# Performance work log

Hardware: AMD Instinct MI355X
Metric: run time of the kernel (lower is better)

## Reference

```python
import jax, jax.numpy as jnp
import numpy as np

HEAD_COUNT = 16
HEAD_DIM = 128  # embed_count // head_count = 2048 // 16


def setup_inputs() -> dict:
    key = jax.random.key(0)
    k0, k1, k2, k3, k4 = jax.random.split(key, 5)
    B, C, S = 4, 2048, 1024
    keys = jax.random.normal(k0, (B, C, 1, S), dtype=jnp.float32)
    values = jax.random.normal(k1, (B, C, 1, S), dtype=jnp.float32)
    queries = jax.random.normal(k2, (B, C, 1, S), dtype=jnp.float32)
    attention_mask = jax.random.randint(k3, (B, S), 0, 2).astype(bool)
    # guarantee at least one valid key per batch row so softmax is finite
    attention_mask = attention_mask.at[:, 0].set(True)
    w_out = jax.random.normal(k4, (C, C), dtype=jnp.float32) * 0.02
    return {"keys": keys, "values": values, "queries": queries,
            "attention_mask": attention_mask, "w_out": w_out}


def reference(keys, values, queries, attention_mask, w_out):
    B, C, _, S = keys.shape
    h, d = HEAD_COUNT, HEAD_DIM
    # keys: [B,C,1,S] -> transpose(1,3) -> [B,S,1,C] -> [B,S,h,d]
    k = jnp.transpose(keys[:, :, 0, :], (0, 2, 1)).reshape(B, S, h, d)      # bkhd
    # values/queries: [B,C,1,S] -> [B,h,d,S] -> transpose(1,2) -> [B,d,h,S]
    v = jnp.transpose(values[:, :, 0, :].reshape(B, h, d, S), (0, 2, 1, 3))  # bdhk
    q = jnp.transpose(queries[:, :, 0, :].reshape(B, h, d, S), (0, 2, 1, 3)) # bdhq
    # additive mask bias: 0 where attended, -inf where masked; broadcast over h,q
    bias = jnp.where(attention_mask, 0.0, -jnp.inf).astype(keys.dtype)       # [B,K]
    scale = 1.0 / np.sqrt(d).astype(np.float32)
    w = jnp.einsum('bdhq,bkhd->bkhq', q * scale, k)                          # [B,K,h,Q]
    w = w + bias[:, :, None, None]
    w = jax.nn.softmax(w, axis=1)  # softmax over keys (dim 1)
    hid = jnp.einsum('bkhq,bdhk->bdhq', w, v)                                # [B,d,h,Q]
    hid = jnp.transpose(hid, (0, 2, 1, 3)).reshape(B, C, S)                  # [B,C,Q]
    out = jnp.einsum('oc,bcq->boq', w_out, hid)                              # 1x1 conv out_proj
    return out.reshape(B, C, 1, S)
```

## Files before the change

kernel.cpp:

```cpp
#include <hip/hip_runtime.h>

#define Bq 4
#define Cc 2048
#define Ss 1024
#define Hh 16
#define Dd 128

#define QSCALE 0.127517429f

typedef __bf16 bf16x8 __attribute__((ext_vector_type(8)));
typedef float  f32x4  __attribute__((ext_vector_type(4)));

__device__ __forceinline__ ushort f2bf(float f) {
    uint u = __float_as_uint(f);
    u += 0x7FFFu + ((u >> 16) & 1u);
    return (ushort)(u >> 16);
}
__device__ __forceinline__ uint pack2bf(float a, float b) {
    return (uint)f2bf(a) | ((uint)f2bf(b) << 16);
}
__device__ __forceinline__ void gld16(const void* g, void* l) {
    __builtin_amdgcn_global_load_lds(
        (const __attribute__((address_space(1))) unsigned int*)g,
        (__attribute__((address_space(3))) unsigned int*)l, 16, 0, 0);
}

__global__ __launch_bounds__(256) void prep_all2(const float* __restrict__ w,
                                                 const float* __restrict__ v,
                                                 const float* __restrict__ keys,
                                                 const float* __restrict__ queries,
                                                 const unsigned* __restrict__ mask,
                                                 ushort* __restrict__ wb,
                                                 ushort* __restrict__ vb,
                                                 ushort* __restrict__ Kt,
                                                 ushort* __restrict__ Qt,
                                                 float* __restrict__ bias) {
    __shared__ __align__(16) float T[128][65];
    const int t = threadIdx.x;
    const int blk = blockIdx.x;

    if (blk < 2048) {
        const size_t e = ((size_t)blk * 256 + t) * 8;
        const int row = (int)(e >> 11), col = (int)(e & 2047);
        const int colS = (col & ~63) | ((col & 63) ^ ((row & 7) << 3));
        float4 v0 = *(const float4*)&w[e];
        float4 v1 = *(const float4*)&w[e + 4];
        uint4 o;
        o.x = pack2bf(v0.x, v0.y); o.y = pack2bf(v0.z, v0.w);
        o.z = pack2bf(v1.x, v1.y); o.w = pack2bf(v1.z, v1.w);
        *(uint4*)&wb[(size_t)row * 2048 + colS] = o;
    } else if (blk < 6144) {
        const int tid = (blk - 2048) * 256 + t;
        const int row = tid >> 7;
        const int cp = tid & 127;
        const int blk64 = (cp >> 3) * 64;
        const int j0 = cp & 7;
        const int b5 = j0 >> 2, h = j0 & 3;
        const float* src = v + (size_t)row * 1024 + blk64 + 32 * b5 + 4 * h;
        float4 A = *(const float4*)src;
        float4 B = *(const float4*)(src + 16);
        uint4 o;
        o.x = pack2bf(A.x, A.y); o.y = pack2bf(A.z, A.w);
        o.z = pack2bf(B.x, B.y); o.w = pack2bf(B.z, B.w);
        *(uint4*)&vb[(size_t)row * 1024 + blk64 + ((j0 * 8) ^ ((row & 7) << 3))] = o;
    } else if (blk < 8192) {
        const int isQ = (blk >= 7168);
        const int b2 = blk - (isQ ? 7168 : 6144);
        const int s0 = (b2 & 15) * 64;
        const int bh = b2 >> 4;
        const float* src = (isQ ? queries : keys) + (size_t)bh * 128 * 1024;
        const float sc = isQ ? QSCALE : 1.0f;
#pragma unroll
        for (int p = 0; p < 8; ++p) {
            const int d = p * 16 + (t >> 4);
            float4 v4 = *(const float4*)&src[(size_t)d * 1024 + s0 + (t & 15) * 4];
            T[d][(t & 15) * 4 + 0] = v4.x * sc;
            T[d][(t & 15) * 4 + 1] = v4.y * sc;
            T[d][(t & 15) * 4 + 2] = v4.z * sc;
            T[d][(t & 15) * 4 + 3] = v4.w * sc;
        }
        __syncthreads();
        ushort* outp = isQ ? Qt : Kt;
#pragma unroll
        for (int p = 0; p < 4; ++p) {
            const int k = p * 16 + (t >> 4);
            const int x = t & 15;
            uint4 o;
            o.x = pack2bf(T[x * 8 + 0][k], T[x * 8 + 1][k]);
            o.y = pack2bf(T[x * 8 + 2][k], T[x * 8 + 3][k]);
            o.z = pack2bf(T[x * 8 + 4][k], T[x * 8 + 5][k]);
            o.w = pack2bf(T[x * 8 + 6][k], T[x * 8 + 7][k]);
            const size_t rowbyte = ((size_t)bh * 1024 + s0 + k) * 256;
            const int boff = isQ ? (x * 16) : ((x * 16) ^ ((k & 7) << 4));
            *(uint4*)((char*)outp + rowbyte + boff) = o;
        }
    } else {
        __shared__ int f01, ff;
        if (t == 0) { f01 = 0; ff = 0; }
        __syncthreads();
        int a = 0, c = 0;
        for (int i = t; i < 1024; i += 256) {
            unsigned vv = mask[i];
            if (vv != 0u && vv != 1u) a = 1;
            if (vv != 0u && vv != 0x3F800000u) c = 1;
        }
        if (a) atomicOr(&f01, 1);
        if (c) atomicOr(&ff, 1);
        __syncthreads();
        const int mode = f01 ? (ff ? 1 : 2) : 0;
        const int* mi = (const int*)mask;
        const unsigned char* mb = (const unsigned char*)mask;
        const float* mf = (const float*)mask;
        for (int i = t; i < Bq * Ss; i += 256) {
            bool on;
            if (mode == 0)      on = (mi[i] != 0);
            else if (mode == 1) on = (mb[i] != 0);
            else                on = (mf[i] != 0.0f);
            bias[i] = on ? 0.0f : -1e30f;
        }
    }
}

__global__ __launch_bounds__(512) void attn9(const ushort* __restrict__ Qt,
                                             const ushort* __restrict__ Kt,
                                             const ushort* __restrict__ Vbf,
                                             const float* __restrict__ bias,
                                             ushort* __restrict__ hidT) {
    __shared__ __align__(16) char SMEM[69632];
    float* biasS = (float*)(SMEM + 65536);

    const int t = threadIdx.x, l = t & 63, w = t >> 6;
    const int kk = l & 15, g = l >> 4;

    const int bid = blockIdx.x;
    const int vid = (bid & 7) * 32 + (bid >> 3);
    const int bh = vid >> 2, qt = vid & 3;
    const int b = bh >> 4, hh = bh & 15;
    const int q0 = qt * 256;
    const size_t bhbase = (size_t)bh * 1024;

    for (int i = t; i < Ss; i += 512) biasS[i] = bias[b * Ss + i];

    bf16x8 qf[2][4];
#pragma unroll
    for (int qs = 0; qs < 2; ++qs) {
        const ushort* qrow = Qt + (bhbase + q0 + w * 32 + qs * 16 + kk) * 128;
#pragma unroll
        for (int dc = 0; dc < 4; ++dc)
            qf[qs][dc] = *(const bf16x8*)(qrow + dc * 32 + g * 8);
    }

    float lrun[2] = {0.0f, 0.0f};
    f32x4 hacc[2][8];
#pragma unroll
    for (int qs = 0; qs < 2; ++qs)
#pragma unroll
        for (int i = 0; i < 8; ++i) hacc[qs][i] = (f32x4){0.f, 0.f, 0.f, 0.f};

#define ATTN_STAGE(bufi, cki)                                                   \
    {                                                                           \
        const int k0n = (cki) * 64;                                             \
        ushort* Kd = (ushort*)SMEM + (bufi) * 8192;                             \
        ushort* Vd = (ushort*)(SMEM + 32768) + (bufi) * 8192;                   \
        _Pragma("unroll")                                                       \
        for (int ii = 0; ii < 4; ++ii) {                                        \
            const int inst = ii * 8 + w;                                        \
            if (inst < 16) {                                                    \
                gld16(Kt + (bhbase + k0n + inst * 4 + (l >> 4)) * 128 +         \
                          (l & 15) * 8,                                         \
                      Kd + inst * 512);                                         \
            } else {                                                            \
                const int i2 = inst - 16;                                       \
                gld16(Vbf + ((size_t)bh * 128 + i2 * 8 + (l >> 3)) * 1024 +     \
                          k0n + (l & 7) * 8,                                    \
                      Vd + i2 * 512);                                           \
            }                                                                   \
        }                                                                       \
    }

#define ATTN_COMPUTE(bi, ck)                                                     \
    {                                                                            \
        const int k0 = (ck) * 64;                                                \
        const ushort* KTb = (const ushort*)SMEM + (bi) * 8192;                   \
        const ushort* Vsb = (const ushort*)(SMEM + 32768) + (bi) * 8192;         \
        f32x4 sc[2][4];                                                          \
        __builtin_amdgcn_s_setprio(1);                                           \
        _Pragma("unroll")                                                        \
        for (int ns = 0; ns < 4; ++ns) {                                         \
            const f32x4 ci = *(const f32x4*)&biasS[k0 + ns * 16 + g * 4];        \
            bf16x8 kf[4];                                                        \
            const ushort* kr = KTb + (ns * 16 + kk) * 128;                       \
            _Pragma("unroll")                                                    \
            for (int dc = 0; dc < 4; ++dc)                                       \
                kf[dc] = *(const bf16x8*)(kr +                                   \
                             ((dc * 32 + g * 8) ^ ((kk & 7) << 3)));             \
            _Pragma("unroll")                                                    \
            for (int qs = 0; qs < 2; ++qs) {                                     \
                f32x4 a = ci;                                                    \
                _Pragma("unroll")                                                \
                for (int dc = 0; dc < 4; ++dc)                                   \
                    a = __builtin_amdgcn_mfma_f32_16x16x32_bf16(                 \
                        kf[dc], qf[qs][dc], a, 0, 0, 0);                         \
                sc[qs][ns] = a;                                                  \
            }                                                                    \
        }                                                                        \
        __builtin_amdgcn_s_setprio(0);                                           \
        bf16x8 pb[2][2];                                                         \
        _Pragma("unroll")                                                        \
        for (int qs = 0; qs < 2; ++qs) {                                         \
            float pv[4][4];                                                      \
            float s = 0.0f;                                                      \
            _Pragma("unroll")                                                    \
            for (int ns = 0; ns < 4; ++ns) {                                     \
                _Pragma("unroll")                                                \
                for (int r = 0; r < 4; ++r) {                                    \
                    float p = exp2f(sc[qs][ns][r]);                              \
                    pv[ns][r] = p;                                               \
                    s += p;                                                      \
                }                                                                \
            }                                                                    \
            lrun[qs] += s;                                                       \
            _Pragma("unroll")                                                    \
            for (int kh = 0; kh < 2; ++kh) {                                     \
                bf16x8 vpk;                                                      \
                _Pragma("unroll")                                                \
                for (int j = 0; j < 8; ++j)                                      \
                    vpk[j] = (__bf16)pv[2 * kh + (j >> 2)][j & 3];               \
                pb[qs][kh] = vpk;                                                \
            }                                                                    \
        }                                                                        \
        __builtin_amdgcn_s_setprio(1);                                           \
        _Pragma("unroll")                                                        \
        for (int kh = 0; kh < 2; ++kh) {                                         \
            _Pragma("unroll")                                                    \
            for (int ds = 0; ds < 8; ++ds) {                                     \
                bf16x8 vf = *(const bf16x8*)(Vsb + (ds * 16 + kk) * 64 +         \
                                 ((kh * 32 + g * 8) ^ ((kk & 7) << 3)));         \
                hacc[0][ds] = __builtin_amdgcn_mfma_f32_16x16x32_bf16(           \
                    vf, pb[0][kh], hacc[0][ds], 0, 0, 0);                        \
                hacc[1][ds] = __builtin_amdgcn_mfma_f32_16x16x32_bf16(           \
                    vf, pb[1][kh], hacc[1][ds], 0, 0, 0);                        \
            }                                                                    \
        }                                                                        \
        __builtin_amdgcn_s_setprio(0);                                           \
    }

    ATTN_STAGE(0, 0);
    asm volatile("s_waitcnt vmcnt(0)" ::: "memory");
    __builtin_amdgcn_s_barrier();

    int buf = 0;
    for (int ck = 0; ck < 16; ++ck) {
        if (ck + 1 < 16) ATTN_STAGE(buf ^ 1, ck + 1);
        ATTN_COMPUTE(buf, ck);
        asm volatile("s_waitcnt vmcnt(0)" ::: "memory");
        __builtin_amdgcn_s_barrier();
        buf ^= 1;
    }
#undef ATTN_STAGE
#undef ATTN_COMPUTE

    float linv[2];
#pragma unroll
    for (int qs = 0; qs < 2; ++qs) {
        float s = lrun[qs];
        s += __shfl_xor(s, 16);
        s += __shfl_xor(s, 32);
        linv[qs] = 1.0f / s;
    }

    __syncthreads();
    {
        ushort* hs = (ushort*)SMEM;
#pragma unroll
        for (int qs = 0; qs < 2; ++qs) {
            const int row = w * 32 + qs * 16 + kk;
#pragma unroll
            for (int ds = 0; ds < 8; ++ds) {
                uint2 pk;
                pk.x = pack2bf(hacc[qs][ds][0] * linv[qs], hacc[qs][ds][1] * linv[qs]);
                pk.y = pack2bf(hacc[qs][ds][2] * linv[qs], hacc[qs][ds][3] * linv[qs]);
                const int off = row * 256 + ((ds * 32 + g * 8) ^ ((row & 7) << 4));
                *(uint2*)((char*)hs + off) = pk;
            }
        }
    }
    __syncthreads();

    const char* hsb = (const char*)SMEM;
#pragma unroll
    for (int it = 0; it < 8; ++it) {
        const int idx = it * 512 + t;
        const int q = idx >> 4, x = idx & 15;
        uint4 vv = *(const uint4*)(hsb + q * 256 + x * 16);
        *(uint4*)((char*)hidT + ((size_t)(b * Ss + q0 + q)) * 4096 + hh * 256 + x * 16) = vv;
    }
}

__global__ __launch_bounds__(512, 2) void proj5(const ushort* __restrict__ Wbf,
                                                const ushort* __restrict__ hidT,
                                                float* __restrict__ out) {
    __shared__ __align__(16) char SMEM[147456];
    const int t = threadIdx.x, l = t & 63, w = t >> 6;
    const int kk = l & 15, g = l >> 4;
    const int wr = w >> 2, wc = w & 3;

    const int bid = blockIdx.x;
    const int vid = (bid & 7) * 32 + (bid >> 3);
    const int o0 = (vid & 15) * 128;
    const int n0 = (vid >> 4) * 256;

    f32x4 acc[4][4];
#pragma unroll
    for (int i = 0; i < 4; ++i)
#pragma unroll
        for (int j = 0; j < 4; ++j) acc[i][j] = (f32x4){0.f, 0.f, 0.f, 0.f};

    const int swz = (kk & 7) << 3;

#define P5_STAGE_A(st, ks)                                                      \
    {                                                                           \
        ushort* Ad = (ushort*)SMEM + (st) * 8192;                               \
        _Pragma("unroll")                                                       \
        for (int ii = 0; ii < 2; ++ii) {                                        \
            const int idx = ii * 512 + t;                                       \
            gld16(Wbf + (size_t)(o0 + (idx >> 3)) * 2048 + (ks) * 64 +          \
                      (idx & 7) * 8,                                            \
                  Ad + idx * 8);                                                \
        }                                                                       \
    }
#define P5_STAGE_B(st, ks, p)                                                   \
    {                                                                           \
        ushort* Bd = (ushort*)(SMEM + 49152) + (st) * 16384;                    \
        _Pragma("unroll")                                                       \
        for (int jj = (p) * 2; jj < (p) * 2 + 2; ++jj) {                        \
            const int idx = jj * 512 + t;                                       \
            gld16(hidT + (size_t)(n0 + (idx >> 3)) * 2048 + (ks) * 64 +         \
                      (idx & 7) * 8,                                            \
                  Bd + idx * 8);                                                \
        }                                                                       \
    }
#define P5_READ(dcv)                                                            \
    _Pragma("unroll")                                                           \
    for (int ms = 0; ms < 4; ++ms)                                              \
        af[ms] = *(const bf16x8*)&Ab[(wr * 64 + ms * 16 + kk) * 64 +            \
                                     (((dcv) * 32 + g * 8) ^ swz)];             \
    _Pragma("unroll")                                                           \
    for (int ns = 0; ns < 4; ++ns)                                              \
        bfr[ns] = *(const bf16x8*)&Bb[(wc * 64 + ns * 16 + kk) * 64 +           \
                                      (((dcv) * 32 + g * 8) ^ swz)];
#define P5_MFMA()                                                               \
    __builtin_amdgcn_s_setprio(1);                                              \
    _Pragma("unroll")                                                           \
    for (int ms = 0; ms < 4; ++ms)                                              \
        _Pragma("unroll")                                                       \
        for (int ns = 0; ns < 4; ++ns)                                          \
            acc[ms][ns] = __builtin_amdgcn_mfma_f32_16x16x32_bf16(              \
                af[ms], bfr[ns], acc[ms][ns], 0, 0, 0);                         \
    __builtin_amdgcn_s_setprio(0);

    P5_STAGE_A(0, 0); P5_STAGE_B(0, 0, 0); P5_STAGE_B(0, 0, 1);
    P5_STAGE_A(1, 1); P5_STAGE_B(1, 1, 0); P5_STAGE_B(1, 1, 1);
    asm volatile("s_waitcnt vmcnt(6)" ::: "memory");
    __builtin_amdgcn_s_barrier();

    int ct = 0, st2 = 2;
    for (int tt = 0; tt < 32; ++tt) {
        const ushort* Ab = (const ushort*)SMEM + ct * 8192;
        const ushort* Bb = (const ushort*)(SMEM + 49152) + ct * 16384;
        bf16x8 af[4], bfr[4];

        P5_READ(0);
        if (tt < 30) { P5_STAGE_A(st2, tt + 2); P5_STAGE_B(st2, tt + 2, 0); }
        __builtin_amdgcn_s_barrier();
        asm volatile("s_waitcnt lgkmcnt(0)" ::: "memory");
        P5_MFMA();
        __builtin_amdgcn_s_barrier();

        P5_READ(1);
        if (tt < 30) P5_STAGE_B(st2, tt + 2, 1);
        if (tt < 30) { asm volatile("s_waitcnt vmcnt(6)" ::: "memory"); }
        else         { asm volatile("s_waitcnt vmcnt(0)" ::: "memory"); }
        __builtin_amdgcn_s_barrier();
        asm volatile("s_waitcnt lgkmcnt(0)" ::: "memory");
        P5_MFMA();
        __builtin_amdgcn_s_barrier();

        ct = (ct == 2) ? 0 : ct + 1;
        st2 = (st2 == 2) ? 0 : st2 + 1;
    }
#undef P5_STAGE_A
#undef P5_STAGE_B
#undef P5_READ
#undef P5_MFMA

#pragma unroll
    for (int ms = 0; ms < 4; ++ms)
#pragma unroll
        for (int ns = 0; ns < 4; ++ns) {
            const int o = o0 + wr * 64 + ms * 16 + g * 4;
            const int n = n0 + wc * 64 + ns * 16 + kk;
            const int bb = n >> 10, qq = n & 1023;
            float* op = out + ((size_t)(bb * Cc + o)) * Ss + qq;
#pragma unroll
            for (int r = 0; r < 4; ++r) op[(size_t)r * Ss] = acc[ms][ns][r];
        }
}

extern "C" void kernel_launch(void* const* d_in, const int* in_sizes, int n_in,
                              void* d_out, int out_size, void* d_ws, size_t ws_size,
                              hipStream_t stream) {
    const float*    keys    = (const float*)d_in[0];
    const float*    values  = (const float*)d_in[1];
    const float*    queries = (const float*)d_in[2];
    const unsigned* mask    = (const unsigned*)d_in[3];
    const float*    w_out   = (const float*)d_in[4];
    float* out = (float*)d_out;

    char* ws = (char*)d_ws;
    float*  bias = (float*)ws;
    ushort* Wbf  = (ushort*)(ws + 16384);
    ushort* Kt   = (ushort*)(ws + 16384 + (8u << 20));
    ushort* Qt   = (ushort*)(ws + 16384 + (24u << 20));
    ushort* Vbf  = (ushort*)(ws + 16384 + (40u << 20));
    ushort* hidT = (ushort*)(ws + 16384 + (56u << 20));

    hipLaunchKernelGGL(prep_all2, dim3(8193), dim3(256), 0, stream,
                       w_out, values, keys, queries, mask,
                       Wbf, Vbf, Kt, Qt, bias);
    hipLaunchKernelGGL(attn9, dim3(256), dim3(512), 0, stream,
                       Qt, Kt, Vbf, bias, hidT);
    hipLaunchKernelGGL(proj5, dim3(256), dim3(512), 0, stream,
                       Wbf, hidT, out);
}
```

Before: 120.9 us.

## Triple-buffer K/V tiles and interleave softmax with PV MFMA in attention

Moves the attention kernel from double to triple buffering of K/V chunks in LDS (shared memory grows to about 100KB), so loads run two chunks ahead and each iteration waits with vmcnt(4) instead of draining all loads. The compute body is also split into halves so softmax of the second half can overlap the PV MFMAs of the first half, and the setprio hints are dropped. The goal is to hide global-load latency and keep the matrix units busier. The cost is more LDS per block, which limits how many blocks fit on a CU.

```diff
diff --git a/kernel.cpp b/kernel.cpp
--- a/kernel.cpp
+++ b/kernel.cpp
@@ -121,13 +121,13 @@
     }
 }
 
-__global__ __launch_bounds__(512) void attn9(const ushort* __restrict__ Qt,
-                                             const ushort* __restrict__ Kt,
-                                             const ushort* __restrict__ Vbf,
-                                             const float* __restrict__ bias,
-                                             ushort* __restrict__ hidT) {
-    __shared__ __align__(16) char SMEM[69632];
-    float* biasS = (float*)(SMEM + 65536);
+__global__ __launch_bounds__(512) void attn10(const ushort* __restrict__ Qt,
+                                              const ushort* __restrict__ Kt,
+                                              const ushort* __restrict__ Vbf,
+                                              const float* __restrict__ bias,
+                                              ushort* __restrict__ hidT) {
+    __shared__ __align__(16) char SMEM[102400];
+    float* biasS = (float*)(SMEM + 98304);
 
     const int t = threadIdx.x, l = t & 63, w = t >> 6;
     const int kk = l & 15, g = l >> 4;
@@ -161,7 +161,7 @@
     {                                                                           \
         const int k0n = (cki) * 64;                                             \
         ushort* Kd = (ushort*)SMEM + (bufi) * 8192;                             \
-        ushort* Vd = (ushort*)(SMEM + 32768) + (bufi) * 8192;                   \
+        ushort* Vd = (ushort*)(SMEM + 49152) + (bufi) * 8192;                   \
         _Pragma("unroll")                                                       \
         for (int ii = 0; ii < 4; ++ii) {                                        \
             const int inst = ii * 8 + w;                                        \
@@ -178,87 +178,95 @@
         }                                                                       \
     }
 
+#define QK_HALF(h)                                                               \
+    _Pragma("unroll")                                                            \
+    for (int n2 = 0; n2 < 2; ++n2) {                                             \
+        const int ns = 2 * (h) + n2;                                             \
+        const f32x4 ci = *(const f32x4*)&biasS[k0 + ns * 16 + g * 4];            \
+        bf16x8 kf[4];                                                            \
+        const ushort* kr = KTb + (ns * 16 + kk) * 128;                           \
+        _Pragma("unroll")                                                        \
+        for (int dc = 0; dc < 4; ++dc)                                           \
+            kf[dc] = *(const bf16x8*)(kr + ((dc * 32 + g * 8) ^ ((kk & 7) << 3)));\
+        _Pragma("unroll")                                                        \
+        for (int qs = 0; qs < 2; ++qs) {                                         \
+            f32x4 a = ci;                                                        \
+            _Pragma("unroll")                                                    \
+            for (int dc = 0; dc < 4; ++dc)                                       \
+                a = __builtin_amdgcn_mfma_f32_16x16x32_bf16(                     \
+                    kf[dc], qf[qs][dc], a, 0, 0, 0);                             \
+            sc[qs][ns] = a;                                                      \
+        }                                                                        \
+    }
+
+#define SM_HALF(h)                                                               \
+    _Pragma("unroll")                                                            \
+    for (int qs = 0; qs < 2; ++qs) {                                             \
+        float pv0[4], pv1[4];                                                    \
+        _Pragma("unroll")                                                        \
+        for (int r = 0; r < 4; ++r) {                                            \
+            pv0[r] = exp2f(sc[qs][2 * (h)][r]);                                  \
+            pv1[r] = exp2f(sc[qs][2 * (h) + 1][r]);                              \
+        }                                                                        \
+        lrun[qs] += (pv0[0] + pv0[1] + pv0[2] + pv0[3])                          \
+                  + (pv1[0] + pv1[1] + pv1[2] + pv1[3]);                         \
+        bf16x8 vpk;                                                              \
+        _Pragma("unroll")                                                        \
+        for (int j = 0; j < 4; ++j) { vpk[j] = (__bf16)pv0[j];                   \
+                                      vpk[j + 4] = (__bf16)pv1[j]; }             \
+        pb[qs][h] = vpk;                                                         \
+    }
+
+#define PV_HALF(h)                                                               \
+    _Pragma("unroll")                                                            \
+    for (int ds = 0; ds < 8; ++ds) {                                             \
+        bf16x8 vf = *(const bf16x8*)(Vsb + (ds * 16 + kk) * 64 +                 \
+                        (((h) * 32 + g * 8) ^ ((kk & 7) << 3)));                 \
+        hacc[0][ds] = __builtin_amdgcn_mfma_f32_16x16x32_bf16(                   \
+            vf, pb[0][h], hacc[0][ds], 0, 0, 0);                                 \
+        hacc[1][ds] = __builtin_amdgcn_mfma_f32_16x16x32_bf16(                   \
+            vf, pb[1][h], hacc[1][ds], 0, 0, 0);                                 \
+    }
+
 #define ATTN_COMPUTE(bi, ck)                                                     \
     {                                                                            \
         const int k0 = (ck) * 64;                                                \
         const ushort* KTb = (const ushort*)SMEM + (bi) * 8192;                   \
-        const ushort* Vsb = (const ushort*)(SMEM + 32768) + (bi) * 8192;         \
+        const ushort* Vsb = (const ushort*)(SMEM + 49152) + (bi) * 8192;         \
         f32x4 sc[2][4];                                                          \
-        __builtin_amdgcn_s_setprio(1);                                           \
-        _Pragma("unroll")                                                        \
-        for (int ns = 0; ns < 4; ++ns) {                                         \
-            const f32x4 ci = *(const f32x4*)&biasS[k0 + ns * 16 + g * 4];        \
-            bf16x8 kf[4];                                                        \
-            const ushort* kr = KTb + (ns * 16 + kk) * 128;                       \
-            _Pragma("unroll")                                                    \
-            for (int dc = 0; dc < 4; ++dc)                                       \
-                kf[dc] = *(const bf16x8*)(kr +                                   \
-                             ((dc * 32 + g * 8) ^ ((kk & 7) << 3)));             \
-            _Pragma("unroll")                                                    \
-            for (int qs = 0; qs < 2; ++qs) {                                     \
-                f32x4 a = ci;                                                    \
-                _Pragma("unroll")                                                \
-                for (int dc = 0; dc < 4; ++dc)                                   \
-                    a = __builtin_amdgcn_mfma_f32_16x16x32_bf16(                 \
-                        kf[dc], qf[qs][dc], a, 0, 0, 0);                         \
-                sc[qs][ns] = a;                                                  \
-            }                                                                    \
-        }                                                                        \
-        __builtin_amdgcn_s_setprio(0);                                           \
         bf16x8 pb[2][2];                                                         \
-        _Pragma("unroll")                                                        \
-        for (int qs = 0; qs < 2; ++qs) {                                         \
-            float pv[4][4];                                                      \
-            float s = 0.0f;                                                      \
-            _Pragma("unroll")                                                    \
-            for (int ns = 0; ns < 4; ++ns) {                                     \
-                _Pragma("unroll")                                                \
-                for (int r = 0; r < 4; ++r) {                                    \
-                    float p = exp2f(sc[qs][ns][r]);                              \
-                    pv[ns][r] = p;                                               \
-                    s += p;                                                      \
-                }                                                                \
-            }                                                                    \
-            lrun[qs] += s;                                                       \
-            _Pragma("unroll")                                                    \
-            for (int kh = 0; kh < 2; ++kh) {                                     \
-                bf16x8 vpk;                                                      \
-                _Pragma("unroll")                                                \
-                for (int j = 0; j < 8; ++j)                                      \
-                    vpk[j] = (__bf16)pv[2 * kh + (j >> 2)][j & 3];               \
-                pb[qs][kh] = vpk;                                                \
-            }                                                                    \
-        }                                                                        \
-        __builtin_amdgcn_s_setprio(1);                                           \
-        _Pragma("unroll")                                                        \
-        for (int kh = 0; kh < 2; ++kh) {                                         \
-            _Pragma("unroll")                                                    \
-            for (int ds = 0; ds < 8; ++ds) {                                     \
-                bf16x8 vf = *(const bf16x8*)(Vsb + (ds * 16 + kk) * 64 +         \
-                                 ((kh * 32 + g * 8) ^ ((kk & 7) << 3)));         \
-                hacc[0][ds] = __builtin_amdgcn_mfma_f32_16x16x32_bf16(           \
-                    vf, pb[0][kh], hacc[0][ds], 0, 0, 0);                        \
-                hacc[1][ds] = __builtin_amdgcn_mfma_f32_16x16x32_bf16(           \
-                    vf, pb[1][kh], hacc[1][ds], 0, 0, 0);                        \
-            }                                                                    \
-        }                                                                        \
-        __builtin_amdgcn_s_setprio(0);                                           \
+        QK_HALF(0);                                                              \
+        QK_HALF(1);                                                              \
+        SM_HALF(0);                             \
+        PV_HALF(0);                                                              \
+        SM_HALF(1);                             \
+        PV_HALF(1);                                                              \
     }
 
     ATTN_STAGE(0, 0);
+    ATTN_STAGE(1, 1);
+    asm volatile("s_waitcnt vmcnt(4)" ::: "memory");
+    __builtin_amdgcn_s_barrier();
+
+    int cb = 0, sb = 2;
+    for (int ck = 0; ck < 14; ++ck) {
+        ATTN_STAGE(sb, ck + 2);
+        ATTN_COMPUTE(cb, ck);
+        asm volatile("s_waitcnt vmcnt(4)" ::: "memory");
+        __builtin_amdgcn_s_barrier();
+        cb = (cb == 2) ? 0 : cb + 1;
+        sb = (sb == 2) ? 0 : sb + 1;
+    }
+    ATTN_COMPUTE(cb, 14);
     asm volatile("s_waitcnt vmcnt(0)" ::: "memory");
     __builtin_amdgcn_s_barrier();
-
-    int buf = 0;
-    for (int ck = 0; ck < 16; ++ck) {
-        if (ck + 1 < 16) ATTN_STAGE(buf ^ 1, ck + 1);
-        ATTN_COMPUTE(buf, ck);
-        asm volatile("s_waitcnt vmcnt(0)" ::: "memory");
-        __builtin_amdgcn_s_barrier();
-        buf ^= 1;
-    }
+    cb = (cb == 2) ? 0 : cb + 1;
+    ATTN_COMPUTE(cb, 15);
 #undef ATTN_STAGE
 #undef ATTN_COMPUTE
+#undef QK_HALF
+#undef SM_HALF
+#undef PV_HALF
 
     float linv[2];
 #pragma unroll
@@ -428,7 +436,7 @@
     hipLaunchKernelGGL(prep_all2, dim3(8193), dim3(256), 0, stream,
                        w_out, values, keys, queries, mask,
                        Wbf, Vbf, Kt, Qt, bias);
-    hipLaunchKernelGGL(attn9, dim3(256), dim3(512), 0, stream,
+    hipLaunchKernelGGL(attn10, dim3(256), dim3(512), 0, stream,
                        Qt, Kt, Vbf, bias, hidT);
     hipLaunchKernelGGL(proj5, dim3(256), dim3(512), 0, stream,
                        Wbf, hidT, out);
```

Result: no change. 119.0 us (-1.5%).
